# Kernel tuning notes

Hardware: AMD Instinct MI355X
Metric: run time of the kernel (lower is better)

The kernel has to match this reference:

```python
import jax, jax.numpy as jnp
import numpy as np

N_NODES = 100000
N_EDGES = 3200000
D_IN = 128
D_HID = 128
N_CLASSES = 40


def setup_inputs() -> dict:
    key = jax.random.key(0)
    ks = jax.random.split(key, 8)
    x = jax.random.normal(ks[0], (N_NODES, D_IN), dtype=jnp.float32)
    edge_index = jax.random.randint(ks[1], (2, N_EDGES), 0, N_NODES, dtype=jnp.int64)
    s1 = 1.0 / np.sqrt(D_IN)
    s2 = 1.0 / np.sqrt(D_HID)
    W1 = jax.random.normal(ks[2], (D_IN, D_HID), dtype=jnp.float32) * s1
    b1 = jnp.zeros((D_HID,), dtype=jnp.float32)
    W2 = jax.random.normal(ks[3], (D_HID, D_HID), dtype=jnp.float32) * s2
    b2 = jnp.zeros((D_HID,), dtype=jnp.float32)
    Wl = jax.random.normal(ks[4], (D_HID, N_CLASSES), dtype=jnp.float32) * s2
    bl = jnp.zeros((N_CLASSES,), dtype=jnp.float32)
    return {"x": x, "edge_index": edge_index, "W1": W1, "b1": b1,
            "W2": W2, "b2": b2, "Wl": Wl, "bl": bl}


def _gcn_conv(x, W, b, src, dst, inv_sqrt_deg, n_nodes):
    # h = X @ W  (linear transform first: cheaper when out_dim <= in_dim)
    h = x @ W  # [N, d_out]
    # symmetric normalization: norm_e = deg(src)^-1/2 * deg(dst)^-1/2
    norm = inv_sqrt_deg[src] * inv_sqrt_deg[dst]  # [E]
    msg = h[src] * norm[:, None]                  # gather + scale  [E, d_out]
    out = jax.ops.segment_sum(msg, dst, num_segments=n_nodes)  # scatter-add
    return out + b


def reference(x, edge_index, W1, b1, W2, b2, Wl, bl):
    n = x.shape[0]
    # GCNConv adds self-loops before normalization (PyG default)
    loops = jnp.arange(n, dtype=edge_index.dtype)
    src = jnp.concatenate([edge_index[0], loops])
    dst = jnp.concatenate([edge_index[1], loops])
    deg = jax.ops.segment_sum(jnp.ones_like(dst, dtype=x.dtype), dst, num_segments=n)
    inv_sqrt_deg = jnp.where(deg > 0, jax.lax.rsqrt(deg), 0.0)

    h = _gcn_conv(x, W1, b1, src, dst, inv_sqrt_deg, n)
    h = jax.nn.relu(h)
    h = _gcn_conv(h, W2, b2, src, dst, inv_sqrt_deg, n)
    h = jax.nn.relu(h)
    return h @ Wl + bl
```

## Files before the change

kernel.cpp:

```cpp
#include <hip/hip_runtime.h>
#include <hip/hip_bf16.h>

typedef _Float16 f16;
typedef _Float16 f16x4 __attribute__((ext_vector_type(4)));
typedef _Float16 f16x8 __attribute__((ext_vector_type(8)));
typedef float f32x4 __attribute__((ext_vector_type(4)));

#define D 128
#define N_CLS 40
#define BN 128
#define NBMAX 1024


__global__ __launch_bounds__(256) void k_hist(const int* __restrict__ dst,
                                              int* __restrict__ bcnt, int e) {
  __shared__ int lh[NBMAX];
  for (int j = threadIdx.x; j < NBMAX; j += 256) lh[j] = 0;
  __syncthreads();
  int stride = gridDim.x * blockDim.x;
  for (int q = blockIdx.x * blockDim.x + threadIdx.x; q < e; q += stride)
    atomicAdd(&lh[dst[q] >> 7], 1);
  __syncthreads();
  for (int j = threadIdx.x; j < NBMAX; j += 256)
    if (lh[j]) atomicAdd(&bcnt[j], lh[j]);
}

__global__ __launch_bounds__(1024) void k_bscan(const int* __restrict__ bcnt,
                                                int* __restrict__ bbase,
                                                int* __restrict__ bcur) {
  __shared__ int sums[NBMAX];
  int t = threadIdx.x;
  int c = bcnt[t];
  sums[t] = c;
  __syncthreads();
  for (int off = 1; off < NBMAX; off <<= 1) {
    int a = (t >= off) ? sums[t - off] : 0;
    __syncthreads();
    sums[t] += a;
    __syncthreads();
  }
  bbase[t] = sums[t] - c;
  bcur[t] = sums[t] - c;
}

__global__ __launch_bounds__(256) void k_place(const int* __restrict__ src,
                                               const int* __restrict__ dst,
                                               int* __restrict__ bcur,
                                               unsigned int* __restrict__ binned,
                                               int e, int nwg) {
  __shared__ int lh[NBMAX];
  __shared__ int lofs[NBMAX];
  __shared__ int lcur[NBMAX];
  int chunk = (e + nwg - 1) / nwg;
  int lo = blockIdx.x * chunk;
  int hi = min(e, lo + chunk);
  int t = threadIdx.x;
  for (int j = t; j < NBMAX; j += 256) { lh[j] = 0; lcur[j] = 0; }
  __syncthreads();
  for (int q = lo + t; q < hi; q += 256) atomicAdd(&lh[dst[q] >> 7], 1);
  __syncthreads();
  for (int j = t; j < NBMAX; j += 256) {
    int c = lh[j];
    lofs[j] = c ? atomicAdd(&bcur[j], c) : 0;
  }
  __syncthreads();
  for (int q = lo + t; q < hi; q += 256) {
    int d = dst[q];
    int b = d >> 7;
    int r = atomicAdd(&lcur[b], 1);
    binned[lofs[b] + r] = ((unsigned int)(d & 127) << 17) | (unsigned int)src[q];
  }
}

__global__ __launch_bounds__(256) void k_csr(const unsigned int* __restrict__ binned,
                                             const int* __restrict__ bbase,
                                             int* __restrict__ csr,
                                             int* __restrict__ deg,
                                             float* __restrict__ isd,
                                             int* __restrict__ row_start, int n) {
  int b = blockIdx.x;
  int lo = bbase[b], hi = bbase[b + 1];
  __shared__ int h[BN];
  __shared__ int sc[BN];
  __shared__ int cur[BN];
  int t = threadIdx.x;
  if (t < BN) h[t] = 0;
  __syncthreads();
  for (int q = lo + t; q < hi; q += 256) atomicAdd(&h[binned[q] >> 17], 1);
  __syncthreads();
  if (t < BN) sc[t] = h[t];
  __syncthreads();
  for (int off = 1; off < BN; off <<= 1) {
    int a = 0;
    if (t < BN && t >= off) a = sc[t - off];
    __syncthreads();
    if (t < BN) sc[t] += a;
    __syncthreads();
  }
  if (t < BN) {
    int excl = sc[t] - h[t];
    cur[t] = lo + excl;
    int i = b * BN + t;
    if (i < n) {
      deg[i] = h[t];
      isd[i] = rsqrtf((float)(h[t] + 1));
      row_start[i] = lo + excl;
    }
  }
  __syncthreads();
  for (int q = lo + t; q < hi; q += 256) {
    unsigned int u = binned[q];
    int p = atomicAdd(&cur[u >> 17], 1);
    csr[p] = (int)(u & 0x1FFFF);
  }
}

template <bool HALF_IN>
__global__ __launch_bounds__(256) void k_gemm_m(const void* __restrict__ Xv,
                                                const float* __restrict__ W,
                                                const float* __restrict__ isd,
                                                f16* __restrict__ HS, int n) {
  __shared__ f16 At[64][136];
  __shared__ f16 Wt[128][136];
  const size_t ss = (size_t)n * 32;
  int t = threadIdx.x;
  int r0 = blockIdx.x * 64;
  if (!HALF_IN) {
    const float* X = (const float*)Xv;
    for (int q = t; q < 64 * 32; q += 256) {
      int row = q >> 5, cb = (q & 31) << 2;
      float4 v = {0.f, 0.f, 0.f, 0.f};
      if (r0 + row < n) v = *(const float4*)(X + (size_t)(r0 + row) * D + cb);
      f16x4 h = {(f16)v.x, (f16)v.y, (f16)v.z, (f16)v.w};
      *(f16x4*)&At[row][cb] = h;
    }
  } else {
    const f16* X = (const f16*)Xv;
    for (int q = t; q < 64 * 16; q += 256) {
      int row = q >> 4, cb = (q & 15) << 3;
      f16x8 v = 0;
      if (r0 + row < n) v = *(const f16x8*)(X + (size_t)(r0 + row) * D + cb);
      *(f16x8*)&At[row][cb] = v;
    }
  }
  for (int q = t; q < (D * D) / 4; q += 256) {
    int k = q >> 5, cq = (q & 31) << 2;
    float4 w = *(const float4*)(W + (size_t)k * D + cq);
    Wt[cq + 0][k] = (f16)w.x;
    Wt[cq + 1][k] = (f16)w.y;
    Wt[cq + 2][k] = (f16)w.z;
    Wt[cq + 3][k] = (f16)w.w;
  }
  __syncthreads();

  int wave = t >> 6, lane = t & 63;
  int lw = lane & 15, kg = lane >> 4;
  f32x4 acc[8];
#pragma unroll
  for (int ct = 0; ct < 8; ++ct) acc[ct] = (f32x4)0.f;
#pragma unroll
  for (int ks = 0; ks < 4; ++ks) {
    f16x8 af = *(const f16x8*)&At[(wave << 4) + lw][ks * 32 + kg * 8];
#pragma unroll
    for (int ct = 0; ct < 8; ++ct) {
      f16x8 bf = *(const f16x8*)&Wt[ct * 16 + lw][ks * 32 + kg * 8];
      acc[ct] = __builtin_amdgcn_mfma_f32_16x16x32_f16(af, bf, acc[ct], 0, 0, 0);
    }
  }
  int rbase = r0 + (wave << 4) + (kg << 2);
  float sv[4];
#pragma unroll
  for (int rr = 0; rr < 4; ++rr)
    sv[rr] = (rbase + rr < n) ? isd[rbase + rr] : 0.f;
#pragma unroll
  for (int ct = 0; ct < 8; ++ct) {
#pragma unroll
    for (int rr = 0; rr < 4; ++rr) {
      int node = rbase + rr;
      if (node < n)
        HS[(size_t)(ct >> 1) * ss + (size_t)node * 32 + ((ct & 1) << 4) + lw] =
            (f16)(acc[ct][rr] * sv[rr]);
    }
  }
}

__device__ inline f16x8 shfl_xor_f16x8(f16x8 v, int m) {
  union { f16x8 h; int i[4]; } u;
  u.h = v;
#pragma unroll
  for (int k = 0; k < 4; ++k) u.i[k] = __shfl_xor(u.i[k], m);
  return u.h;
}

__global__ __launch_bounds__(256) void k_aggs(const f16* __restrict__ HS,
                                              const int* __restrict__ csr,
                                              const int* __restrict__ row_start,
                                              const int* __restrict__ deg,
                                              const float* __restrict__ bias,
                                              f16* __restrict__ G, int n) {
  const size_t ss = (size_t)n * 32;
  int t = threadIdx.x;
  int wave = t >> 6, lane = t & 63;
  int g = lane >> 4, r = lane & 15;
  int s = blockIdx.x & 3;
  int i0 = ((blockIdx.x >> 2) << 4) + (wave << 2) + g;
  bool ok = i0 < n;
  int i = ok ? i0 : n - 1;
  int q = r & 3, er = r >> 2;
  int dg = deg[i];
  const int* cp = csr + row_start[i];
  const char* sbase = (const char*)(HS + (size_t)s * ss);
  unsigned qofs = (unsigned)(q << 4);
  f16x8 a0 = (f16x8)0, a1 = (f16x8)0, a2 = (f16x8)0, a3 = (f16x8)0;
  int iA = cp[er];
  int iB = cp[er + 4];
  int iC = cp[er + 8];
  int iD = cp[er + 12];
  for (int u = 0; u < dg; u += 16) {
    unsigned oA = ((unsigned)iA << 6) + qofs;
    unsigned oB = ((unsigned)iB << 6) + qofs;
    unsigned oC = ((unsigned)iC << 6) + qofs;
    unsigned oD = ((unsigned)iD << 6) + qofs;
    iA = cp[u + 16 + er];
    iB = cp[u + 20 + er];
    iC = cp[u + 24 + er];
    iD = cp[u + 28 + er];
    if (u + er < dg)
      a0 += *(const f16x8*)(sbase + oA);
    if (u + 4 + er < dg)
      a1 += *(const f16x8*)(sbase + oB);
    if (u + 8 + er < dg)
      a2 += *(const f16x8*)(sbase + oC);
    if (u + 12 + er < dg)
      a3 += *(const f16x8*)(sbase + oD);
  }
  f16x8 tv = (a0 + a1) + (a2 + a3);
  tv += shfl_xor_f16x8(tv, 4);
  tv += shfl_xor_f16x8(tv, 8);
  f16x8 svv = *(const f16x8*)(sbase + ((unsigned)i << 6) + qofs);
  float di = rsqrtf((float)(dg + 1));
  const float* bp = bias + s * 32 + (q << 3);
  float4 b0 = *(const float4*)bp;
  float4 b1 = *(const float4*)(bp + 4);
  float bv[8] = {b0.x, b0.y, b0.z, b0.w, b1.x, b1.y, b1.z, b1.w};
  f16x8 ov;
#pragma unroll
  for (int j = 0; j < 8; ++j) {
    float v = di * ((float)tv[j] + (float)svv[j]) + bv[j];
    v = v > 0.f ? v : 0.f;
    ov[j] = (f16)v;
  }
  if (ok && er == 0)
    *(f16x8*)(G + (size_t)i * D + s * 32 + (q << 3)) = ov;
}

__global__ __launch_bounds__(256) void k_cls(const f16* __restrict__ H,
                                             const float* __restrict__ Wl,
                                             const float* __restrict__ bl,
                                             float* __restrict__ out, int n) {
  __shared__ float wt[N_CLS][D];
  int t = threadIdx.x;
  for (int q = t; q < D * N_CLS; q += 256) {
    int k = q / N_CLS, c = q - k * N_CLS;
    wt[c][k] = Wl[q];
  }
  int wv = t >> 6, lane = t & 63, g = lane >> 4, l = lane & 15;
  float bb0 = bl[l];
  float bb1 = bl[16 + l];
  float bb2 = (l < 8) ? bl[32 + l] : 0.f;
  __syncthreads();
  int node0 = (blockIdx.x << 7) + (wv << 2) + g;
  for (int it = 0; it < 8; ++it) {
    int node = node0 + it * 16;
    if (node >= n) break;
    f16x8 h = *(const f16x8*)(H + (size_t)node * D + l * 8);
    float hf[8];
#pragma unroll
    for (int j = 0; j < 8; ++j) hf[j] = (float)h[j];
    float r0 = bb0, r1 = bb1, r2 = bb2;
#pragma unroll 4
    for (int c = 0; c < N_CLS; ++c) {
      const float* wp = &wt[c][l * 8];
      float4 w0 = *(const float4*)wp;
      float4 w1 = *(const float4*)(wp + 4);
      float p = hf[0] * w0.x + hf[1] * w0.y + hf[2] * w0.z + hf[3] * w0.w +
                hf[4] * w1.x + hf[5] * w1.y + hf[6] * w1.z + hf[7] * w1.w;
      p += __shfl_xor(p, 1);
      p += __shfl_xor(p, 2);
      p += __shfl_xor(p, 4);
      p += __shfl_xor(p, 8);
      if ((c & 15) == l) {
        if (c < 16) r0 += p;
        else if (c < 32) r1 += p;
        else r2 += p;
      }
    }
    float* op = out + (size_t)node * N_CLS;
    op[l] = r0;
    op[16 + l] = r1;
    if (l < 8) op[32 + l] = r2;
  }
}

extern "C" void kernel_launch(void* const* d_in, const int* in_sizes, int n_in,
                              void* d_out, int out_size, void* d_ws, size_t ws_size,
                              hipStream_t stream) {
  const float* x  = (const float*)d_in[0];
  const int*   ei = (const int*)d_in[1];
  const float* W1 = (const float*)d_in[2];
  const float* b1 = (const float*)d_in[3];
  const float* W2 = (const float*)d_in[4];
  const float* b2 = (const float*)d_in[5];
  const float* Wl = (const float*)d_in[6];
  const float* bl = (const float*)d_in[7];
  float* out = (float*)d_out;

  const int n = in_sizes[0] / D;
  const int e = in_sizes[1] / 2;
  const int* src = ei;
  const int* dst = ei + e;
  const int nb = (n + BN - 1) / BN;

  char* ws = (char*)d_ws;
  size_t off = 0;
  auto alloc = [&](size_t bytes) -> void* {
    void* p = ws + off;
    off += (bytes + 255) & ~(size_t)255;
    return p;
  };
  int*   bcnt      = (int*)alloc(NBMAX * 4);
  int*   bbase     = (int*)alloc(NBMAX * 4);
  int*   bcur      = (int*)alloc(NBMAX * 4);
  int*   deg       = (int*)alloc((size_t)n * 4);
  int*   row_start = (int*)alloc((size_t)n * 4);
  float* isd       = (float*)alloc((size_t)n * 4);
  int*   csr       = (int*)alloc(((size_t)e + 64) * 4);
  f16*   hA        = (f16*)alloc((size_t)n * D * 2);
  f16*   hB        = (f16*)alloc((size_t)n * D * 2);
  unsigned int* binned = (unsigned int*)hA;

  hipMemsetAsync(bcnt, 0, NBMAX * 4, stream);
  hipMemsetAsync(csr + e, 0, 64 * 4, stream);

  const int nwg_place = 512;
  k_hist<<<1024, 256, 0, stream>>>(dst, bcnt, e);
  k_bscan<<<1, 1024, 0, stream>>>(bcnt, bbase, bcur);
  k_place<<<nwg_place, 256, 0, stream>>>(src, dst, bcur, binned, e, nwg_place);
  k_csr<<<nb, 256, 0, stream>>>(binned, bbase, csr, deg, isd, row_start, n);

  int gblocks = (n + 63) / 64;
  int ablocks = ((n + 15) / 16) * 4;
  k_gemm_m<false><<<gblocks, 256, 0, stream>>>(x, W1, isd, hA, n);
  k_aggs<<<ablocks, 256, 0, stream>>>(hA, csr, row_start, deg, b1, hB, n);
  k_gemm_m<true><<<gblocks, 256, 0, stream>>>(hB, W2, isd, hA, n);
  k_aggs<<<ablocks, 256, 0, stream>>>(hA, csr, row_start, deg, b2, hB, n);
  k_cls<<<(n + 127) / 128, 256, 0, stream>>>(hB, Wl, bl, out, n);
}
```

Baseline: 646.3 us.

## Pretranspose weights once, load A fragments directly, stage GEMM output through LDS

```diff
diff --git a/kernel.cpp b/kernel.cpp
--- a/kernel.cpp
+++ b/kernel.cpp
@@ -115,71 +115,86 @@
   }
 }
 
+__global__ __launch_bounds__(256) void k_wt(const float* __restrict__ W1,
+                                            const float* __restrict__ W2,
+                                            f16* __restrict__ O1,
+                                            f16* __restrict__ O2) {
+  const float* W = blockIdx.x ? W2 : W1;
+  f16* O = blockIdx.x ? O2 : O1;
+  __shared__ f16 lt[D][136];
+  int t = threadIdx.x;
+  for (int q = t; q < D * D; q += 256) {
+    int k = q >> 7, c = q & 127;
+    lt[c][k] = (f16)W[q];
+  }
+  __syncthreads();
+  for (int q = t; q < D * 16; q += 256) {
+    int row = q >> 4, cb = (q & 15) << 3;
+    *(f16x8*)(O + ((size_t)row << 7) + cb) = *(const f16x8*)&lt[row][cb];
+  }
+}
+
 template <bool HALF_IN>
 __global__ __launch_bounds__(256) void k_gemm_m(const void* __restrict__ Xv,
-                                                const float* __restrict__ W,
+                                                const f16* __restrict__ Wtr,
                                                 const float* __restrict__ isd,
                                                 f16* __restrict__ HS, int n) {
-  __shared__ f16 At[64][136];
-  __shared__ f16 Wt[128][136];
+  __shared__ f16 Wt[D][136];
+  __shared__ f16 ot[64][136];
   const size_t ss = (size_t)n * 32;
   int t = threadIdx.x;
   int r0 = blockIdx.x * 64;
-  if (!HALF_IN) {
-    const float* X = (const float*)Xv;
-    for (int q = t; q < 64 * 32; q += 256) {
-      int row = q >> 5, cb = (q & 31) << 2;
-      float4 v = {0.f, 0.f, 0.f, 0.f};
-      if (r0 + row < n) v = *(const float4*)(X + (size_t)(r0 + row) * D + cb);
-      f16x4 h = {(f16)v.x, (f16)v.y, (f16)v.z, (f16)v.w};
-      *(f16x4*)&At[row][cb] = h;
-    }
-  } else {
-    const f16* X = (const f16*)Xv;
-    for (int q = t; q < 64 * 16; q += 256) {
-      int row = q >> 4, cb = (q & 15) << 3;
-      f16x8 v = 0;
-      if (r0 + row < n) v = *(const f16x8*)(X + (size_t)(r0 + row) * D + cb);
-      *(f16x8*)&At[row][cb] = v;
-    }
-  }
-  for (int q = t; q < (D * D) / 4; q += 256) {
-    int k = q >> 5, cq = (q & 31) << 2;
-    float4 w = *(const float4*)(W + (size_t)k * D + cq);
-    Wt[cq + 0][k] = (f16)w.x;
-    Wt[cq + 1][k] = (f16)w.y;
-    Wt[cq + 2][k] = (f16)w.z;
-    Wt[cq + 3][k] = (f16)w.w;
+  for (int q = t; q < D * 16; q += 256) {
+    int row = q >> 4, cb = (q & 15) << 3;
+    *(f16x8*)&Wt[row][cb] = *(const f16x8*)(Wtr + ((size_t)row << 7) + cb);
   }
   __syncthreads();
 
   int wave = t >> 6, lane = t & 63;
   int lw = lane & 15, kg = lane >> 4;
+  int arow = r0 + (wave << 4) + lw;
+  if (arow >= n) arow = n - 1;
   f32x4 acc[8];
 #pragma unroll
   for (int ct = 0; ct < 8; ++ct) acc[ct] = (f32x4)0.f;
 #pragma unroll
   for (int ks = 0; ks < 4; ++ks) {
-    f16x8 af = *(const f16x8*)&At[(wave << 4) + lw][ks * 32 + kg * 8];
+    f16x8 af;
+    if (HALF_IN) {
+      af = *(const f16x8*)((const f16*)Xv + (size_t)arow * D + ks * 32 + kg * 8);
+    } else {
+      const float* xp = (const float*)Xv + (size_t)arow * D + ks * 32 + kg * 8;
+      float4 x0 = *(const float4*)xp;
+      float4 x1 = *(const float4*)(xp + 4);
+      af[0] = (f16)x0.x; af[1] = (f16)x0.y; af[2] = (f16)x0.z; af[3] = (f16)x0.w;
+      af[4] = (f16)x1.x; af[5] = (f16)x1.y; af[6] = (f16)x1.z; af[7] = (f16)x1.w;
+    }
 #pragma unroll
     for (int ct = 0; ct < 8; ++ct) {
       f16x8 bf = *(const f16x8*)&Wt[ct * 16 + lw][ks * 32 + kg * 8];
       acc[ct] = __builtin_amdgcn_mfma_f32_16x16x32_f16(af, bf, acc[ct], 0, 0, 0);
     }
   }
-  int rbase = r0 + (wave << 4) + (kg << 2);
+  int lrow = (wave << 4) + (kg << 2);
   float sv[4];
 #pragma unroll
-  for (int rr = 0; rr < 4; ++rr)
-    sv[rr] = (rbase + rr < n) ? isd[rbase + rr] : 0.f;
-#pragma unroll
-  for (int ct = 0; ct < 8; ++ct) {
-#pragma unroll
-    for (int rr = 0; rr < 4; ++rr) {
-      int node = rbase + rr;
-      if (node < n)
-        HS[(size_t)(ct >> 1) * ss + (size_t)node * 32 + ((ct & 1) << 4) + lw] =
-            (f16)(acc[ct][rr] * sv[rr]);
+  for (int rr = 0; rr < 4; ++rr) {
+    int node = r0 + lrow + rr;
+    sv[rr] = isd[node < n ? node : n - 1];
+  }
+#pragma unroll
+  for (int ct = 0; ct < 8; ++ct)
+#pragma unroll
+    for (int rr = 0; rr < 4; ++rr)
+      ot[lrow + rr][ct * 16 + lw] = (f16)(acc[ct][rr] * sv[rr]);
+  __syncthreads();
+  {
+    int orow = t >> 2, cb = (t & 3) << 3;
+    if (r0 + orow < n) {
+#pragma unroll
+      for (int s = 0; s < 4; ++s)
+        *(f16x8*)(HS + (size_t)s * ss + (size_t)(r0 + orow) * 32 + cb) =
+            *(const f16x8*)&ot[orow][s * 32 + cb];
     }
   }
 }
@@ -335,6 +350,8 @@
   int*   row_start = (int*)alloc((size_t)n * 4);
   float* isd       = (float*)alloc((size_t)n * 4);
   int*   csr       = (int*)alloc(((size_t)e + 64) * 4);
+  f16*   Wt1       = (f16*)alloc((size_t)D * D * 2);
+  f16*   Wt2       = (f16*)alloc((size_t)D * D * 2);
   f16*   hA        = (f16*)alloc((size_t)n * D * 2);
   f16*   hB        = (f16*)alloc((size_t)n * D * 2);
   unsigned int* binned = (unsigned int*)hA;
@@ -347,12 +364,13 @@
   k_bscan<<<1, 1024, 0, stream>>>(bcnt, bbase, bcur);
   k_place<<<nwg_place, 256, 0, stream>>>(src, dst, bcur, binned, e, nwg_place);
   k_csr<<<nb, 256, 0, stream>>>(binned, bbase, csr, deg, isd, row_start, n);
+  k_wt<<<2, 256, 0, stream>>>(W1, W2, Wt1, Wt2);
 
   int gblocks = (n + 63) / 64;
   int ablocks = ((n + 15) / 16) * 4;
-  k_gemm_m<false><<<gblocks, 256, 0, stream>>>(x, W1, isd, hA, n);
+  k_gemm_m<false><<<gblocks, 256, 0, stream>>>(x, Wt1, isd, hA, n);
   k_aggs<<<ablocks, 256, 0, stream>>>(hA, csr, row_start, deg, b1, hB, n);
-  k_gemm_m<true><<<gblocks, 256, 0, stream>>>(hB, W2, isd, hA, n);
+  k_gemm_m<true><<<gblocks, 256, 0, stream>>>(hB, Wt2, isd, hA, n);
   k_aggs<<<ablocks, 256, 0, stream>>>(hA, csr, row_start, deg, b2, hB, n);
   k_cls<<<(n + 127) / 128, 256, 0, stream>>>(hB, Wl, bl, out, n);
 }
```

Measured after the change: 594.7 us. 8.0% less time.
